# Optimization experiments

Measured on AMD Instinct MI355X. Metric: run time of the kernel, lower is better.

The kernel has to match this reference:

```python
import jax, jax.numpy as jnp
import numpy as np

N_NODES = 100000
N_EDGES = 1600000
NODE_F = 8   # augmented node features
EDGE_F = 2   # augmented edge features
GLOB_F = 1
HID = 16
L = 3        # message passing steps

EDGE_IN = GLOB_F + EDGE_F + 2 * NODE_F   # 19
NODE_IN = GLOB_F + EDGE_F + NODE_F       # 11
GLOB_IN = EDGE_F + NODE_F + GLOB_F       # 11


def setup_inputs() -> dict:
    key = jax.random.key(0)
    ks = jax.random.split(key, 20)
    inp = {
        "x": jax.random.normal(ks[0], (N_NODES, NODE_F), dtype=jnp.float32),
        "edge_index": jax.random.randint(ks[1], (2, N_EDGES), 0, N_NODES, dtype=jnp.int32),
        "edge_attr": jax.random.normal(ks[2], (N_EDGES, EDGE_F), dtype=jnp.float32),
        "g": jax.random.normal(ks[3], (1, GLOB_F), dtype=jnp.float32),
    }
    s = 0.1
    inp["edge_W1"] = jax.random.normal(ks[4], (L, EDGE_IN, HID), dtype=jnp.float32) * s
    inp["edge_b1"] = jnp.zeros((L, HID), dtype=jnp.float32)
    inp["edge_W2"] = jax.random.normal(ks[5], (L, HID, EDGE_F), dtype=jnp.float32) * s
    inp["edge_b2"] = jnp.zeros((L, EDGE_F), dtype=jnp.float32)
    inp["node_W1"] = jax.random.normal(ks[6], (L, NODE_IN, HID), dtype=jnp.float32) * s
    inp["node_b1"] = jnp.zeros((L, HID), dtype=jnp.float32)
    inp["node_W2"] = jax.random.normal(ks[7], (L, HID, NODE_F), dtype=jnp.float32) * s
    inp["node_b2"] = jnp.zeros((L, NODE_F), dtype=jnp.float32)
    inp["glob_W1"] = jax.random.normal(ks[8], (L, GLOB_IN, HID), dtype=jnp.float32) * s
    inp["glob_b1"] = jnp.zeros((L, HID), dtype=jnp.float32)
    inp["glob_W2"] = jax.random.normal(ks[9], (L, HID, GLOB_F), dtype=jnp.float32) * s
    inp["glob_b2"] = jnp.zeros((L, GLOB_F), dtype=jnp.float32)
    return inp


def _mlp(h, W1, b1, W2, b2):
    # two-layer MLP with ReLU after first layer only (activate_final=False, no layer_norm)
    return jnp.maximum(h @ W1 + b1, 0.0) @ W2 + b2


def reference(x, edge_index, edge_attr, g,
              edge_W1, edge_b1, edge_W2, edge_b2,
              node_W1, node_b1, node_W2, node_b2,
              glob_W1, glob_b1, glob_W2, glob_b2):
    row, col = edge_index[0], edge_index[1]
    n = x.shape[0]
    for l in range(L):
        g_e = jnp.broadcast_to(g, (row.shape[0], GLOB_F))
        # edge block: gather node features along edges, concat, MLP -> [E, EDGE_F]
        e_in = jnp.concatenate([g_e, x[row], x[col], edge_attr], axis=1)
        edge_emb = _mlp(e_in, edge_W1[l], edge_b1[l], edge_W2[l], edge_b2[l])
        # sum-aggregate edge embeddings to source nodes
        agg = jax.ops.segment_sum(edge_emb, row, num_segments=n)
        g_n = jnp.broadcast_to(g, (n, GLOB_F))
        node_emb = _mlp(jnp.concatenate([g_n, x, agg], axis=1),
                        node_W1[l], node_b1[l], node_W2[l], node_b2[l])
        # global block on mean-aggregated edge/node embeddings
        edge_gl = jnp.mean(edge_emb, axis=0, keepdims=True)
        node_gl = jnp.mean(node_emb, axis=0, keepdims=True)
        g = _mlp(jnp.concatenate([node_gl, edge_gl, g], axis=1),
                 glob_W1[l], glob_b1[l], glob_W2[l], glob_b2[l])
        x, edge_attr = node_emb, edge_emb
    return x  # final node embeddings [N, NODE_F]
```

## Files before the change

kernel.cpp:

```cpp
#include <hip/hip_runtime.h>

#define NN 100000
#define NE 1600000
#define CH 4096
#define NCHUNK ((NE + CH - 1) / CH)
#define NBUCK ((NN + 255) / 256)
#define ECHUNK 1024

__device__ __forceinline__ float wave_red(float v) {
#pragma unroll
    for (int off = 32; off > 0; off >>= 1) v += __shfl_down(v, off, 64);
    return v;
}

__device__ __forceinline__ void stage16(void* lds, const void* gsrc) {
    __builtin_amdgcn_global_load_lds(
        (const __attribute__((address_space(1))) unsigned int*)gsrc,
        (__attribute__((address_space(3))) unsigned int*)lds,
        16, 0, 0);
}

__global__ __launch_bounds__(256) void hist_kernel(
    const int* __restrict__ ei, int* __restrict__ hist)
{
    __shared__ int h[NBUCK];
    int t = threadIdx.x, c = blockIdx.x;
    for (int b = t; b < NBUCK; b += 256) h[b] = 0;
    __syncthreads();
    int base = c * CH;
    for (int i = t; i < CH; i += 256) {
        int e = base + i;
        if (e < NE) atomicAdd(&h[ei[e] >> 8], 1);
    }
    __syncthreads();
    for (int b = t; b < NBUCK; b += 256) hist[c * NBUCK + b] = h[b];
}

__global__ __launch_bounds__(512) void bscan_kernel(
    const int* __restrict__ hist, int* __restrict__ baseT, int* __restrict__ colTotal)
{
    __shared__ int buf[2][512];
    int b = blockIdx.x, t = threadIdx.x;
    int v = (t < NCHUNK) ? hist[t * NBUCK + b] : 0;
    buf[0][t] = v;
    __syncthreads();
    int src = 0;
    for (int d = 1; d < 512; d <<= 1) {
        int nv = buf[src][t] + ((t >= d) ? buf[src][t - d] : 0);
        buf[src ^ 1][t] = nv;
        src ^= 1;
        __syncthreads();
    }
    if (t < NCHUNK) baseT[b * NCHUNK + t] = buf[src][t] - v;
    if (t == NCHUNK - 1) colTotal[b] = buf[src][t];
}

__global__ __launch_bounds__(512) void boff_kernel(
    const int* __restrict__ colTotal, int* __restrict__ b_off)
{
    __shared__ int buf[2][512];
    int t = threadIdx.x;
    int v = (t < NBUCK) ? colTotal[t] : 0;
    buf[0][t] = v;
    __syncthreads();
    int src = 0;
    for (int d = 1; d < 512; d <<= 1) {
        int nv = buf[src][t] + ((t >= d) ? buf[src][t - d] : 0);
        buf[src ^ 1][t] = nv;
        src ^= 1;
        __syncthreads();
    }
    if (t < NBUCK) b_off[t] = buf[src][t] - v;
    if (t == NBUCK - 1) b_off[NBUCK] = buf[src][t];
}

__global__ __launch_bounds__(256) void fillb_kernel(
    const int* __restrict__ ei, const float* __restrict__ eattr,
    const int* __restrict__ baseT, const int* __restrict__ b_off,
    int* __restrict__ keys, float2* __restrict__ attrS)
{
    __shared__ int sslot[NBUCK];
    int t = threadIdx.x, c = blockIdx.x;
    for (int b = t; b < NBUCK; b += 256)
        sslot[b] = b_off[b] + baseT[b * NCHUNK + c];
    __syncthreads();
    int base = c * CH;
    for (int i = t; i < CH; i += 256) {
        int e = base + i;
        if (e < NE) {
            int row = ei[e];
            int slot = atomicAdd(&sslot[row >> 8], 1);
            keys[slot] = ((row & 255) << 17) | ei[NE + e];
            attrS[slot] = reinterpret_cast<const float2*>(eattr)[e];
        }
    }
}

template <bool WRITE_EMB, bool NEED_SUM>
__global__ __launch_bounds__(512, 4) void fused_kernel(
    const int* __restrict__ keys,
    const float2* __restrict__ ein, float2* __restrict__ eout,
    const int* __restrict__ b_off,
    const float* __restrict__ gptr,
    const float* __restrict__ eW1, const float* __restrict__ eB1,
    const float* __restrict__ eW2, const float* __restrict__ eB2,
    const float* __restrict__ xin,
    const float* __restrict__ nW1, const float* __restrict__ nB1,
    const float* __restrict__ nW2, const float* __restrict__ nB2,
    float* __restrict__ xout, float* __restrict__ sums)
{
    __shared__ float  sPr[256][20];
    __shared__ float  sagg[256][2];
    __shared__ int    kbuf[2][ECHUNK];
    __shared__ float2 abuf[2][ECHUNK];
    __shared__ float  redE[8][2];
    __shared__ float  redN[4][8];
    int tid = threadIdx.x;
    ((float*)sagg)[tid] = 0.f;

    int n0 = blockIdx.x * 256;
    float gval = gptr[0];
    bool own = (tid < 256) && (n0 + tid < NN);
    float xv[8];
    if (own) {
        const float4* xi = reinterpret_cast<const float4*>(xin + (size_t)(n0 + tid) * 8);
        float4 a0 = xi[0], a1 = xi[1];
        xv[0] = a0.x; xv[1] = a0.y; xv[2] = a0.z; xv[3] = a0.w;
        xv[4] = a1.x; xv[5] = a1.y; xv[6] = a1.z; xv[7] = a1.w;
        float pr[16];
#pragma unroll
        for (int q = 0; q < 16; q++) pr[q] = 0.f;
#pragma unroll
        for (int k = 0; k < 8; k++) {
            float v = xv[k];
#pragma unroll
            for (int q = 0; q < 16; q++) pr[q] += v * eW1[(1 + k) * 16 + q];
        }
        float4* pw = reinterpret_cast<float4*>(&sPr[tid][0]);
#pragma unroll
        for (int t4 = 0; t4 < 4; t4++)
            pw[t4] = make_float4(pr[4*t4], pr[4*t4+1], pr[4*t4+2], pr[4*t4+3]);
    }

    int e0 = b_off[blockIdx.x], e1 = b_off[blockIdx.x + 1];
    int a0 = e0 & ~3;
    int nc = (e1 - a0 + ECHUNK - 1) / ECHUNK;

    if (tid < 256) stage16(&kbuf[0][tid * 4], keys + a0 + tid * 4);
    stage16(&abuf[0][tid * 2], ein + a0 + tid * 2);

    float gterm[16];
#pragma unroll
    for (int q = 0; q < 16; q++) gterm[q] = eB1[q] + gval * eW1[q];

    float t0 = 0.f, t1 = 0.f;
    for (int c = 0; c < nc; c++) {
        __syncthreads();
        int cur = c & 1;
        if (c + 1 < nc) {
            int wb = a0 + (c + 1) * ECHUNK;
            if (tid < 256) stage16(&kbuf[cur ^ 1][tid * 4], keys + wb + tid * 4);
            stage16(&abuf[cur ^ 1][tid * 2], ein + wb + tid * 2);
        }
        int cbase = a0 + c * ECHUNK;
#pragma unroll
        for (int j = 0; j < 2; j++) {
            int idx = tid + j * 512;
            int e = cbase + idx;
            if (e < e0 || e >= e1) continue;
            int k = kbuf[cur][idx];
            float2 ea = abuf[cur][idx];
            int li = k >> 17, col = k & 0x1FFFF;
            const float4* xc4 = reinterpret_cast<const float4*>(xin + (size_t)col * 8);
            float4 c0 = xc4[0], c1 = xc4[1];
            const float4* pr4 = reinterpret_cast<const float4*>(&sPr[li][0]);
            float4 p0 = pr4[0], p1 = pr4[1], p2 = pr4[2], p3 = pr4[3];
            float h[16];
            h[0]  = gterm[0]  + p0.x; h[1]  = gterm[1]  + p0.y;
            h[2]  = gterm[2]  + p0.z; h[3]  = gterm[3]  + p0.w;
            h[4]  = gterm[4]  + p1.x; h[5]  = gterm[5]  + p1.y;
            h[6]  = gterm[6]  + p1.z; h[7]  = gterm[7]  + p1.w;
            h[8]  = gterm[8]  + p2.x; h[9]  = gterm[9]  + p2.y;
            h[10] = gterm[10] + p2.z; h[11] = gterm[11] + p2.w;
            h[12] = gterm[12] + p3.x; h[13] = gterm[13] + p3.y;
            h[14] = gterm[14] + p3.z; h[15] = gterm[15] + p3.w;
            float xc[8] = {c0.x, c0.y, c0.z, c0.w, c1.x, c1.y, c1.z, c1.w};
#pragma unroll
            for (int kk = 0; kk < 8; kk++) {
                float v = xc[kk];
#pragma unroll
                for (int q = 0; q < 16; q++) h[q] += v * eW1[(9 + kk) * 16 + q];
            }
#pragma unroll
            for (int q = 0; q < 16; q++) {
                h[q] += ea.x * eW1[17 * 16 + q];
                h[q] += ea.y * eW1[18 * 16 + q];
            }
            float s0 = eB2[0], s1 = eB2[1];
#pragma unroll
            for (int q = 0; q < 16; q++) {
                float rr = fmaxf(h[q], 0.f);
                s0 += rr * eW2[2 * q];
                s1 += rr * eW2[2 * q + 1];
            }
            if (WRITE_EMB) eout[e] = make_float2(s0, s1);
            atomicAdd(&sagg[li][0], s0);
            atomicAdd(&sagg[li][1], s1);
            t0 += s0; t1 += s1;
        }
    }

    if (NEED_SUM) {
        float r0 = wave_red(t0), r1 = wave_red(t1);
        int wave = tid >> 6, lane = tid & 63;
        if (lane == 0) { redE[wave][0] = r0; redE[wave][1] = r1; }
    }
    __syncthreads();
    if (NEED_SUM && tid == 0) {
        float s0 = 0.f, s1 = 0.f;
#pragma unroll
        for (int w = 0; w < 8; w++) { s0 += redE[w][0]; s1 += redE[w][1]; }
        atomicAdd(&sums[0], s0);
        atomicAdd(&sums[1], s1);
    }

    float out[8];
#pragma unroll
    for (int m = 0; m < 8; m++) out[m] = 0.f;

    if (own) {
        int n = n0 + tid;
        float in[11];
        in[0] = gval;
#pragma unroll
        for (int k = 0; k < 8; k++) in[1 + k] = xv[k];
        in[9] = sagg[tid][0]; in[10] = sagg[tid][1];

        float h[16];
#pragma unroll
        for (int q = 0; q < 16; q++) h[q] = nB1[q];
#pragma unroll
        for (int k = 0; k < 11; k++) {
            float v = in[k];
#pragma unroll
            for (int q = 0; q < 16; q++) h[q] += v * nW1[k * 16 + q];
        }
#pragma unroll
        for (int m = 0; m < 8; m++) out[m] = nB2[m];
#pragma unroll
        for (int q = 0; q < 16; q++) {
            float hq = fmaxf(h[q], 0.f);
#pragma unroll
            for (int m = 0; m < 8; m++) out[m] += hq * nW2[q * 8 + m];
        }
        float4* xo = reinterpret_cast<float4*>(xout + (size_t)n * 8);
        xo[0] = make_float4(out[0], out[1], out[2], out[3]);
        xo[1] = make_float4(out[4], out[5], out[6], out[7]);
    }
    if (NEED_SUM) {
        float r[8];
#pragma unroll
        for (int m = 0; m < 8; m++) r[m] = wave_red(out[m]);
        int wave = tid >> 6, lane = tid & 63;
        if (wave < 4 && lane == 0) {
#pragma unroll
            for (int m = 0; m < 8; m++) redN[wave][m] = r[m];
        }
        __syncthreads();
        if (tid == 0) {
#pragma unroll
            for (int m = 0; m < 8; m++) {
                float s = redN[0][m] + redN[1][m] + redN[2][m] + redN[3][m];
                atomicAdd(&sums[2 + m], s);
            }
        }
    }
}

__global__ void glob_kernel(const float* __restrict__ sums,
                            const float* __restrict__ gold,
                            const float* __restrict__ W1, const float* __restrict__ B1,
                            const float* __restrict__ W2, const float* __restrict__ B2,
                            float* __restrict__ gnew)
{
    if (threadIdx.x == 0 && blockIdx.x == 0) {
        float in[11];
#pragma unroll
        for (int j = 0; j < 8; j++) in[j] = sums[2 + j] * (1.0f / NN);
        in[8] = sums[0] * (1.0f / NE);
        in[9] = sums[1] * (1.0f / NE);
        in[10] = gold[0];
        float acc = B2[0];
#pragma unroll
        for (int j = 0; j < 16; j++) {
            float h = B1[j];
#pragma unroll
            for (int k = 0; k < 11; k++) h += in[k] * W1[k * 16 + j];
            acc += fmaxf(h, 0.f) * W2[j];
        }
        gnew[0] = acc;
    }
}

extern "C" void kernel_launch(void* const* d_in, const int* in_sizes, int n_in,
                              void* d_out, int out_size, void* d_ws, size_t ws_size,
                              hipStream_t stream) {
    const float* x     = (const float*)d_in[0];
    const int*   ei    = (const int*)d_in[1];
    const float* eattr = (const float*)d_in[2];
    const float* g     = (const float*)d_in[3];
    const float* eW1 = (const float*)d_in[4];
    const float* eB1 = (const float*)d_in[5];
    const float* eW2 = (const float*)d_in[6];
    const float* eB2 = (const float*)d_in[7];
    const float* nW1 = (const float*)d_in[8];
    const float* nB1 = (const float*)d_in[9];
    const float* nW2 = (const float*)d_in[10];
    const float* nB2 = (const float*)d_in[11];
    const float* gW1 = (const float*)d_in[12];
    const float* gB1 = (const float*)d_in[13];
    const float* gW2 = (const float*)d_in[14];
    const float* gB2 = (const float*)d_in[15];
    float* out = (float*)d_out;

    char* ws = (char*)d_ws;
    float*  xb0   = (float*)(ws);
    float*  xb1   = (float*)(ws + 3200000);
    int*    b_off = (int*)  (ws + 6400000);
    float*  sums  = (float*)(ws + 6401600);
    float*  g1    = (float*)(ws + 6401728);
    float*  g2    = g1 + 1;
    int*    keys  = (int*)  (ws + 6401792);
    float2* attrS = (float2*)(ws + 12809984);
    float2* eembS = (float2*)(ws + 25626368);
    int*    hist     = (int*)xb1;
    int*    baseT    = (int*)((char*)xb1 + 611584);
    int*    colTotal = (int*)((char*)xb1 + 1223168);

    dim3 blk(256);
    dim3 fblk(512);
    dim3 cgrid(NCHUNK);
    dim3 bgrid(NBUCK);

    hipMemsetAsync(sums, 0, 128, stream);
    hist_kernel<<<cgrid, blk, 0, stream>>>(ei, hist);
    bscan_kernel<<<bgrid, 512, 0, stream>>>(hist, baseT, colTotal);
    boff_kernel<<<1, 512, 0, stream>>>(colTotal, b_off);
    fillb_kernel<<<cgrid, blk, 0, stream>>>(ei, eattr, baseT, b_off, keys, attrS);

    fused_kernel<true, true><<<bgrid, fblk, 0, stream>>>(
        keys, attrS, eembS, b_off, g,
        eW1, eB1, eW2, eB2,
        x, nW1, nB1, nW2, nB2,
        xb0, sums);
    glob_kernel<<<1, 64, 0, stream>>>(sums, g, gW1, gB1, gW2, gB2, g1);

    fused_kernel<true, true><<<bgrid, fblk, 0, stream>>>(
        keys, eembS, eembS, b_off, g1,
        eW1 + 304, eB1 + 16, eW2 + 32, eB2 + 2,
        xb0, nW1 + 176, nB1 + 16, nW2 + 128, nB2 + 8,
        xb1, sums + 16);
    glob_kernel<<<1, 64, 0, stream>>>(sums + 16, g1, gW1 + 176, gB1 + 16, gW2 + 16, gB2 + 1, g2);

    fused_kernel<false, false><<<bgrid, fblk, 0, stream>>>(
        keys, eembS, nullptr, b_off, g2,
        eW1 + 608, eB1 + 32, eW2 + 64, eB2 + 4,
        xb1, nW1 + 352, nB1 + 32, nW2 + 256, nB2 + 16,
        out, sums);
}
```

Baseline: 343.3 us.

## Split neighbour gather into separate high-parallelism kernel and pack edge records

Packs key and edge attributes into one 16-byte record per edge, with the edge embedding written back in place. Adds a separate gather kernel that copies the destination-node features for every sorted edge into contiguous arrays, using four independent loads per thread so many random reads are in flight at once. The fused kernel then reads only streaming data plus LDS, and drops the LDS double-buffered staging. The cost is extra global traffic: about 51 MB of gathered features written and read back per layer, plus wider records.

```diff
diff --git a/kernel.cpp b/kernel.cpp
--- a/kernel.cpp
+++ b/kernel.cpp
@@ -5,19 +5,13 @@
 #define CH 4096
 #define NCHUNK ((NE + CH - 1) / CH)
 #define NBUCK ((NN + 255) / 256)
-#define ECHUNK 1024
+#define GGRID 1563
+#define GT (GGRID * 256)
 
 __device__ __forceinline__ float wave_red(float v) {
 #pragma unroll
     for (int off = 32; off > 0; off >>= 1) v += __shfl_down(v, off, 64);
     return v;
-}
-
-__device__ __forceinline__ void stage16(void* lds, const void* gsrc) {
-    __builtin_amdgcn_global_load_lds(
-        (const __attribute__((address_space(1))) unsigned int*)gsrc,
-        (__attribute__((address_space(3))) unsigned int*)lds,
-        16, 0, 0);
 }
 
 __global__ __launch_bounds__(256) void hist_kernel(
@@ -77,7 +71,7 @@
 __global__ __launch_bounds__(256) void fillb_kernel(
     const int* __restrict__ ei, const float* __restrict__ eattr,
     const int* __restrict__ baseT, const int* __restrict__ b_off,
-    int* __restrict__ keys, float2* __restrict__ attrS)
+    float4* __restrict__ rec)
 {
     __shared__ int sslot[NBUCK];
     int t = threadIdx.x, c = blockIdx.x;
@@ -90,16 +84,49 @@
         if (e < NE) {
             int row = ei[e];
             int slot = atomicAdd(&sslot[row >> 8], 1);
-            keys[slot] = ((row & 255) << 17) | ei[NE + e];
-            attrS[slot] = reinterpret_cast<const float2*>(eattr)[e];
+            float2 ea = reinterpret_cast<const float2*>(eattr)[e];
+            float4 v;
+            v.x = __int_as_float(((row & 255) << 17) | ei[NE + e]);
+            v.y = 0.f; v.z = ea.x; v.w = ea.y;
+            rec[slot] = v;
+        }
+    }
+}
+
+__global__ __launch_bounds__(256) void gathx_kernel(
+    const float4* __restrict__ rec, const float* __restrict__ xin,
+    float4* __restrict__ gA, float4* __restrict__ gB)
+{
+    int t = blockIdx.x * 256 + threadIdx.x;
+    bool v[4]; float4 r[4];
+#pragma unroll
+    for (int k = 0; k < 4; k++) {
+        int s = t + k * GT;
+        v[k] = (s < NE);
+        if (v[k]) r[k] = rec[s];
+    }
+    float4 a[4], b[4];
+#pragma unroll
+    for (int k = 0; k < 4; k++) {
+        if (v[k]) {
+            int col = __float_as_int(r[k].x) & 0x1FFFF;
+            const float4* p = reinterpret_cast<const float4*>(xin + (size_t)col * 8);
+            a[k] = p[0]; b[k] = p[1];
+        }
+    }
+#pragma unroll
+    for (int k = 0; k < 4; k++) {
+        if (v[k]) {
+            int s = t + k * GT;
+            gA[s] = a[k]; gB[s] = b[k];
         }
     }
 }
 
 template <bool WRITE_EMB, bool NEED_SUM>
-__global__ __launch_bounds__(512, 4) void fused_kernel(
-    const int* __restrict__ keys,
-    const float2* __restrict__ ein, float2* __restrict__ eout,
+__global__ __launch_bounds__(512) void fused_kernel(
+    float4* __restrict__ rec,
+    const float4* __restrict__ gA, const float4* __restrict__ gB,
     const int* __restrict__ b_off,
     const float* __restrict__ gptr,
     const float* __restrict__ eW1, const float* __restrict__ eB1,
@@ -109,12 +136,10 @@
     const float* __restrict__ nW2, const float* __restrict__ nB2,
     float* __restrict__ xout, float* __restrict__ sums)
 {
-    __shared__ float  sPr[256][20];
-    __shared__ float  sagg[256][2];
-    __shared__ int    kbuf[2][ECHUNK];
-    __shared__ float2 abuf[2][ECHUNK];
-    __shared__ float  redE[8][2];
-    __shared__ float  redN[4][8];
+    __shared__ float sPr[256][20];
+    __shared__ float sagg[256][2];
+    __shared__ float redE[8][2];
+    __shared__ float redN[4][8];
     int tid = threadIdx.x;
     ((float*)sagg)[tid] = 0.f;
 
@@ -141,73 +166,57 @@
         for (int t4 = 0; t4 < 4; t4++)
             pw[t4] = make_float4(pr[4*t4], pr[4*t4+1], pr[4*t4+2], pr[4*t4+3]);
     }
+    __syncthreads();
 
     int e0 = b_off[blockIdx.x], e1 = b_off[blockIdx.x + 1];
-    int a0 = e0 & ~3;
-    int nc = (e1 - a0 + ECHUNK - 1) / ECHUNK;
-
-    if (tid < 256) stage16(&kbuf[0][tid * 4], keys + a0 + tid * 4);
-    stage16(&abuf[0][tid * 2], ein + a0 + tid * 2);
 
     float gterm[16];
 #pragma unroll
     for (int q = 0; q < 16; q++) gterm[q] = eB1[q] + gval * eW1[q];
 
     float t0 = 0.f, t1 = 0.f;
-    for (int c = 0; c < nc; c++) {
-        __syncthreads();
-        int cur = c & 1;
-        if (c + 1 < nc) {
-            int wb = a0 + (c + 1) * ECHUNK;
-            if (tid < 256) stage16(&kbuf[cur ^ 1][tid * 4], keys + wb + tid * 4);
-            stage16(&abuf[cur ^ 1][tid * 2], ein + wb + tid * 2);
-        }
-        int cbase = a0 + c * ECHUNK;
-#pragma unroll
-        for (int j = 0; j < 2; j++) {
-            int idx = tid + j * 512;
-            int e = cbase + idx;
-            if (e < e0 || e >= e1) continue;
-            int k = kbuf[cur][idx];
-            float2 ea = abuf[cur][idx];
-            int li = k >> 17, col = k & 0x1FFFF;
-            const float4* xc4 = reinterpret_cast<const float4*>(xin + (size_t)col * 8);
-            float4 c0 = xc4[0], c1 = xc4[1];
-            const float4* pr4 = reinterpret_cast<const float4*>(&sPr[li][0]);
-            float4 p0 = pr4[0], p1 = pr4[1], p2 = pr4[2], p3 = pr4[3];
-            float h[16];
-            h[0]  = gterm[0]  + p0.x; h[1]  = gterm[1]  + p0.y;
-            h[2]  = gterm[2]  + p0.z; h[3]  = gterm[3]  + p0.w;
-            h[4]  = gterm[4]  + p1.x; h[5]  = gterm[5]  + p1.y;
-            h[6]  = gterm[6]  + p1.z; h[7]  = gterm[7]  + p1.w;
-            h[8]  = gterm[8]  + p2.x; h[9]  = gterm[9]  + p2.y;
-            h[10] = gterm[10] + p2.z; h[11] = gterm[11] + p2.w;
-            h[12] = gterm[12] + p3.x; h[13] = gterm[13] + p3.y;
-            h[14] = gterm[14] + p3.z; h[15] = gterm[15] + p3.w;
-            float xc[8] = {c0.x, c0.y, c0.z, c0.w, c1.x, c1.y, c1.z, c1.w};
-#pragma unroll
-            for (int kk = 0; kk < 8; kk++) {
-                float v = xc[kk];
-#pragma unroll
-                for (int q = 0; q < 16; q++) h[q] += v * eW1[(9 + kk) * 16 + q];
-            }
-#pragma unroll
-            for (int q = 0; q < 16; q++) {
-                h[q] += ea.x * eW1[17 * 16 + q];
-                h[q] += ea.y * eW1[18 * 16 + q];
-            }
-            float s0 = eB2[0], s1 = eB2[1];
-#pragma unroll
-            for (int q = 0; q < 16; q++) {
-                float rr = fmaxf(h[q], 0.f);
-                s0 += rr * eW2[2 * q];
-                s1 += rr * eW2[2 * q + 1];
-            }
-            if (WRITE_EMB) eout[e] = make_float2(s0, s1);
-            atomicAdd(&sagg[li][0], s0);
-            atomicAdd(&sagg[li][1], s1);
-            t0 += s0; t1 += s1;
-        }
+    for (int e = e0 + tid; e < e1; e += 512) {
+        float4 r  = rec[e];
+        float4 ca = gA[e];
+        float4 cb = gB[e];
+        int key = __float_as_int(r.x);
+        int li  = key >> 17;
+        float ea0 = r.z, ea1 = r.w;
+        const float4* pr4 = reinterpret_cast<const float4*>(&sPr[li][0]);
+        float4 p0 = pr4[0], p1 = pr4[1], p2 = pr4[2], p3 = pr4[3];
+        float h[16];
+        h[0]  = gterm[0]  + p0.x; h[1]  = gterm[1]  + p0.y;
+        h[2]  = gterm[2]  + p0.z; h[3]  = gterm[3]  + p0.w;
+        h[4]  = gterm[4]  + p1.x; h[5]  = gterm[5]  + p1.y;
+        h[6]  = gterm[6]  + p1.z; h[7]  = gterm[7]  + p1.w;
+        h[8]  = gterm[8]  + p2.x; h[9]  = gterm[9]  + p2.y;
+        h[10] = gterm[10] + p2.z; h[11] = gterm[11] + p2.w;
+        h[12] = gterm[12] + p3.x; h[13] = gterm[13] + p3.y;
+        h[14] = gterm[14] + p3.z; h[15] = gterm[15] + p3.w;
+        float xc[8] = {ca.x, ca.y, ca.z, ca.w, cb.x, cb.y, cb.z, cb.w};
+#pragma unroll
+        for (int kk = 0; kk < 8; kk++) {
+            float v = xc[kk];
+#pragma unroll
+            for (int q = 0; q < 16; q++) h[q] += v * eW1[(9 + kk) * 16 + q];
+        }
+#pragma unroll
+        for (int q = 0; q < 16; q++) {
+            h[q] += ea0 * eW1[17 * 16 + q];
+            h[q] += ea1 * eW1[18 * 16 + q];
+        }
+        float s0 = eB2[0], s1 = eB2[1];
+#pragma unroll
+        for (int q = 0; q < 16; q++) {
+            float rr = fmaxf(h[q], 0.f);
+            s0 += rr * eW2[2 * q];
+            s1 += rr * eW2[2 * q + 1];
+        }
+        if (WRITE_EMB)
+            reinterpret_cast<float2*>(rec)[2 * e + 1] = make_float2(s0, s1);
+        atomicAdd(&sagg[li][0], s0);
+        atomicAdd(&sagg[li][1], s1);
+        t0 += s0; t1 += s1;
     }
 
     if (NEED_SUM) {
@@ -330,9 +339,9 @@
     float*  sums  = (float*)(ws + 6401600);
     float*  g1    = (float*)(ws + 6401728);
     float*  g2    = g1 + 1;
-    int*    keys  = (int*)  (ws + 6401792);
-    float2* attrS = (float2*)(ws + 12809984);
-    float2* eembS = (float2*)(ws + 25626368);
+    float4* rec   = (float4*)(ws + 6401792);
+    float4* gA    = (float4*)(ws + 32001792);
+    float4* gB    = (float4*)(ws + 57601792);
     int*    hist     = (int*)xb1;
     int*    baseT    = (int*)((char*)xb1 + 611584);
     int*    colTotal = (int*)((char*)xb1 + 1223168);
@@ -341,29 +350,33 @@
     dim3 fblk(512);
     dim3 cgrid(NCHUNK);
     dim3 bgrid(NBUCK);
+    dim3 ggrid(GGRID);
 
     hipMemsetAsync(sums, 0, 128, stream);
     hist_kernel<<<cgrid, blk, 0, stream>>>(ei, hist);
     bscan_kernel<<<bgrid, 512, 0, stream>>>(hist, baseT, colTotal);
     boff_kernel<<<1, 512, 0, stream>>>(colTotal, b_off);
-    fillb_kernel<<<cgrid, blk, 0, stream>>>(ei, eattr, baseT, b_off, keys, attrS);
-
+    fillb_kernel<<<cgrid, blk, 0, stream>>>(ei, eattr, baseT, b_off, rec);
+
+    gathx_kernel<<<ggrid, blk, 0, stream>>>(rec, x, gA, gB);
     fused_kernel<true, true><<<bgrid, fblk, 0, stream>>>(
-        keys, attrS, eembS, b_off, g,
+        rec, gA, gB, b_off, g,
         eW1, eB1, eW2, eB2,
         x, nW1, nB1, nW2, nB2,
         xb0, sums);
     glob_kernel<<<1, 64, 0, stream>>>(sums, g, gW1, gB1, gW2, gB2, g1);
 
+    gathx_kernel<<<ggrid, blk, 0, stream>>>(rec, xb0, gA, gB);
     fused_kernel<true, true><<<bgrid, fblk, 0, stream>>>(
-        keys, eembS, eembS, b_off, g1,
+        rec, gA, gB, b_off, g1,
         eW1 + 304, eB1 + 16, eW2 + 32, eB2 + 2,
         xb0, nW1 + 176, nB1 + 16, nW2 + 128, nB2 + 8,
         xb1, sums + 16);
     glob_kernel<<<1, 64, 0, stream>>>(sums + 16, g1, gW1 + 176, gB1 + 16, gW2 + 16, gB2 + 1, g2);
 
+    gathx_kernel<<<ggrid, blk, 0, stream>>>(rec, xb1, gA, gB);
     fused_kernel<false, false><<<bgrid, fblk, 0, stream>>>(
-        keys, eembS, nullptr, b_off, g2,
+        rec, gA, gB, b_off, g2,
         eW1 + 608, eB1 + 32, eW2 + 64, eB2 + 4,
         xb1, nW1 + 352, nB1 + 32, nW2 + 256, nB2 + 16,
         out, sums);
```

Result: slower. 507.2 us (+47.7%).
